# Performance work log

Hardware: AMD Instinct MI355X
Metric: run time of the kernel (lower is better)

## Reference

```python
import jax, jax.numpy as jnp
import numpy as np

D_IN = 512
D_OUT = 512


def setup_inputs() -> dict:
    key = jax.random.key(0)
    ks = jax.random.split(key, 7)
    B, S = 4, 4096
    sc = 1.0 / np.sqrt(D_IN)
    return {
        "x": jax.random.normal(ks[0], (B, S, D_IN), dtype=jnp.float32),
        "Wq": jax.random.normal(ks[1], (D_IN, D_OUT), dtype=jnp.float32) * sc,
        "bq": jnp.zeros((D_OUT,), dtype=jnp.float32),
        "Wk": jax.random.normal(ks[2], (D_IN, D_OUT), dtype=jnp.float32) * sc,
        "bk": jnp.zeros((D_OUT,), dtype=jnp.float32),
        "Wv": jax.random.normal(ks[3], (D_IN, D_OUT), dtype=jnp.float32) * sc,
        "bv": jnp.zeros((D_OUT,), dtype=jnp.float32),
    }


def reference(x, Wq, bq, Wk, bk, Wv, bv):
    # Linear projections
    Q = x @ Wq + bq  # [B,S,Do]
    K = x @ Wk + bk
    V = x @ Wv + bv
    # NOTE: original torch code computes `len(K) ** 1 / 2` which is
    # (len(K)**1)/2 = batch_size / 2 due to operator precedence (not sqrt).
    scale = x.shape[0] / 2.0
    scores = jnp.einsum("bsd,btd->bst", Q, K) / scale  # [B,S,S]
    a = jax.nn.softmax(scores, axis=-1)
    Z = jnp.einsum("bst,btd->bsd", a, V)  # [B,S,Do]
    return Z
```

## Files before the change

### kernel.cpp

```cpp
#include <hip/hip_runtime.h>

typedef _Float16 h8 __attribute__((ext_vector_type(8)));
typedef float f4 __attribute__((ext_vector_type(4)));

#define MFMA16(a, b, c) __builtin_amdgcn_mfma_f32_16x16x32_f16((a), (b), (c), 0, 0, 0)

__device__ static inline void gl_lds16(const void* g, void* l) {
  __builtin_amdgcn_global_load_lds((const __attribute__((address_space(1))) unsigned int*)g,
                                   (__attribute__((address_space(3))) unsigned int*)l, 16, 0, 0);
}

__device__ static inline unsigned encf(float f) {
  unsigned u = __float_as_uint(f);
  return (u & 0x80000000u) ? ~u : (u | 0x80000000u);
}
__device__ static inline float decf(unsigned u) {
  return __uint_as_float((u & 0x80000000u) ? (u ^ 0x80000000u) : ~u);
}


__global__ void wconv_kernel(const float* __restrict__ Wq, const float* __restrict__ Wk,
                             const float* __restrict__ Wv, _Float16* __restrict__ Wt,
                             unsigned* __restrict__ mEnc) {
  int idx = blockIdx.x * 256 + threadIdx.x;
  if (idx < 16384) mEnc[idx] = 0u;
  int z = idx >> 15, rem = idx & 32767;
  int n = rem >> 6, k0 = (rem & 63) << 3;
  const float* W = (z == 0) ? Wq : (z == 1) ? Wk : Wv;
  float sc = (z == 0) ? 0.5f : 1.0f;
  h8 v;
#pragma unroll
  for (int j = 0; j < 8; ++j) v[j] = (_Float16)(W[(k0 + j) * 512 + n] * sc);
  size_t blk = (size_t)((z * 4 + (n >> 7)) * 8 + (k0 >> 6));
  int off = (n & 127) * 64 + ((((k0 >> 3) & 7) ^ (n & 7)) << 3);
  *(h8*)&Wt[blk * 8192 + off] = v;
}

__global__ void xconv_kernel(const float* __restrict__ x, _Float16* __restrict__ Ximg) {
  int idx = blockIdx.x * 256 + threadIdx.x;
  int row = idx >> 6;
  int k0 = (idx & 63) << 3;
  const float* src = &x[(size_t)row * 512 + k0];
  float4 f0 = *(const float4*)src, f1 = *(const float4*)(src + 4);
  h8 v;
  v[0] = (_Float16)f0.x; v[1] = (_Float16)f0.y; v[2] = (_Float16)f0.z; v[3] = (_Float16)f0.w;
  v[4] = (_Float16)f1.x; v[5] = (_Float16)f1.y; v[6] = (_Float16)f1.z; v[7] = (_Float16)f1.w;
  size_t blk = (size_t)((row >> 7) * 8 + (k0 >> 6));
  int off = (row & 127) * 64 + ((((k0 >> 3) & 7) ^ (row & 7)) << 3);
  *(h8*)&Ximg[blk * 8192 + off] = v;
}

__global__ __launch_bounds__(256, 3)
void proj_kernel(const _Float16* __restrict__ Ximg, const _Float16* __restrict__ Wt,
                 const float* __restrict__ bq, const float* __restrict__ bk,
                 const float* __restrict__ bv,
                 char* __restrict__ Qimg, char* __restrict__ Kimg, char* __restrict__ VTimg) {
  __shared__ _Float16 sMem[16384];
  _Float16* sA = sMem;
  _Float16* sB = sMem + 8192;
  const int tid = threadIdx.x;
  const int wave = tid >> 6, lane = tid & 63;
  const int quad = lane >> 4, lr = lane & 15;
  const int nb4 = blockIdx.x;
  const int mb = blockIdx.y;
  const int z = blockIdx.z;
  const int mbase = mb * 128, nbase = nb4 * 128;
  const int rbase = (wave & 1) * 64, cbase = (wave >> 1) * 64;
  const char* Ab = (const char*)Ximg + ((size_t)(mb * 8)) * 16384;
  const char* Bb = (const char*)Wt + ((size_t)((z * 4 + nb4) * 8)) * 16384;

  f4 acc[4][4];
#pragma unroll
  for (int i = 0; i < 4; ++i)
#pragma unroll
    for (int j = 0; j < 4; ++j) { f4 zz = {0.f, 0.f, 0.f, 0.f}; acc[i][j] = zz; }

#pragma unroll
  for (int j = 0; j < 4; ++j) {
    gl_lds16(Ab + tid * 16 + j * 4096, (char*)sA + tid * 16 + j * 4096);
    gl_lds16(Bb + tid * 16 + j * 4096, (char*)sB + tid * 16 + j * 4096);
  }

  for (int kt = 0; kt < 8; ++kt) {
    asm volatile("s_waitcnt vmcnt(0)" ::: "memory");
    __builtin_amdgcn_s_barrier();
    __builtin_amdgcn_sched_barrier(0);
    h8 a[4][2], bb[4][2];
#pragma unroll
    for (int ks = 0; ks < 2; ++ks) {
#pragma unroll
      for (int rt = 0; rt < 4; ++rt) {
        const int r = rbase + rt * 16 + lr;
        a[rt][ks] = *(const h8*)&sA[r * 64 + ((((ks << 2) | quad) ^ (lr & 7)) << 3)];
      }
#pragma unroll
      for (int ct = 0; ct < 4; ++ct) {
        const int r = cbase + ct * 16 + lr;
        bb[ct][ks] = *(const h8*)&sB[r * 64 + ((((ks << 2) | quad) ^ (lr & 7)) << 3)];
      }
    }
    asm volatile("s_waitcnt lgkmcnt(0)" ::: "memory");
    __builtin_amdgcn_s_barrier();
    __builtin_amdgcn_sched_barrier(0);
    if (kt < 7) {
#pragma unroll
      for (int j = 0; j < 4; ++j) {
        gl_lds16(Ab + (kt + 1) * 16384 + tid * 16 + j * 4096, (char*)sA + tid * 16 + j * 4096);
        gl_lds16(Bb + (kt + 1) * 16384 + tid * 16 + j * 4096, (char*)sB + tid * 16 + j * 4096);
      }
    }
    __builtin_amdgcn_s_setprio(1);
#pragma unroll
    for (int ks = 0; ks < 2; ++ks)
#pragma unroll
      for (int rt = 0; rt < 4; ++rt)
#pragma unroll
        for (int ct = 0; ct < 4; ++ct)
          acc[rt][ct] = MFMA16(a[rt][ks], bb[ct][ks], acc[rt][ct]);
    __builtin_amdgcn_s_setprio(0);
  }

  const float* bias = (z == 0) ? bq : (z == 1) ? bk : bv;
  const float bscale = (z == 0) ? 0.5f : 1.0f;
  _Float16* sC = sMem;
  __syncthreads();
#pragma unroll
  for (int ct = 0; ct < 4; ++ct) {
    const int dl = cbase + ct * 16 + lr;
    const float bb = bias[nbase + dl] * bscale;
#pragma unroll
    for (int rt = 0; rt < 4; ++rt) {
#pragma unroll
      for (int r = 0; r < 4; ++r) {
        const int sl = rbase + rt * 16 + quad * 4 + r;
        const _Float16 val = (_Float16)(acc[rt][ct][r] + bb);
        if (z == 2) {
          sC[((sl >> 6) << 13) + dl * 64 + ((((sl >> 3) & 7) ^ (dl & 7)) << 3) + (sl & 7)] = val;
        } else {
          sC[((dl >> 6) << 13) + sl * 64 + ((((dl >> 3) & 7) ^ (sl & 7)) << 3) + (dl & 7)] = val;
        }
      }
    }
  }
  __syncthreads();
  const int b_ = mbase >> 12;
  char* dst;
  if (z != 2) {
    char* img = (z == 0) ? Qimg : Kimg;
    dst = img + ((size_t)((b_ * 32 + ((mbase & 4095) >> 7)) * 8 + (nbase >> 6) + (tid >> 7))) * 16384;
  } else {
    dst = VTimg + ((size_t)((b_ * 4 + (nbase >> 7)) * 64 + ((mbase & 4095) >> 6) + (tid >> 7))) * 16384;
  }
  dst += (size_t)(tid & 127) * 128;
#pragma unroll
  for (int k = 0; k < 8; ++k)
    *(int4*)(dst + k * 16) = *(const int4*)&sC[tid * 64 + k * 8];
}

__global__ __launch_bounds__(256, 3)
void qk_kernel(const char* __restrict__ Qimg, const char* __restrict__ Kimg,
               char* __restrict__ S, unsigned* __restrict__ mEnc, int b0, int s0) {
  __shared__ _Float16 sMem[16384];
  _Float16* sA = sMem;
  _Float16* sB = sMem + 8192;
  const int tid = threadIdx.x;
  const int wave = tid >> 6, lane = tid & 63;
  const int quad = lane >> 4, lr = lane & 15;
  const int cb = blockIdx.x;
  const int rbL = blockIdx.z * gridDim.y + blockIdx.y;
  const int b = b0 + blockIdx.z;
  const int rbase = (wave & 1) * 64, cbase = (wave >> 1) * 64;
  const char* Ab = Qimg + ((size_t)((b * 32 + (s0 >> 7) + blockIdx.y) * 8)) * 16384;
  const char* Bb = Kimg + ((size_t)((b * 32 + cb) * 8)) * 16384;

  f4 acc[4][4];
#pragma unroll
  for (int i = 0; i < 4; ++i)
#pragma unroll
    for (int j = 0; j < 4; ++j) { f4 zz = {0.f, 0.f, 0.f, 0.f}; acc[i][j] = zz; }

#pragma unroll
  for (int j = 0; j < 4; ++j) {
    gl_lds16(Ab + tid * 16 + j * 4096, (char*)sA + tid * 16 + j * 4096);
    gl_lds16(Bb + tid * 16 + j * 4096, (char*)sB + tid * 16 + j * 4096);
  }

  for (int kt = 0; kt < 8; ++kt) {
    asm volatile("s_waitcnt vmcnt(0)" ::: "memory");
    __builtin_amdgcn_s_barrier();
    __builtin_amdgcn_sched_barrier(0);
    h8 a[4][2], bb[4][2];
#pragma unroll
    for (int ks = 0; ks < 2; ++ks) {
#pragma unroll
      for (int rt = 0; rt < 4; ++rt) {
        const int r = rbase + rt * 16 + lr;
        a[rt][ks] = *(const h8*)&sA[r * 64 + ((((ks << 2) | quad) ^ (lr & 7)) << 3)];
      }
#pragma unroll
      for (int ct = 0; ct < 4; ++ct) {
        const int r = cbase + ct * 16 + lr;
        bb[ct][ks] = *(const h8*)&sB[r * 64 + ((((ks << 2) | quad) ^ (lr & 7)) << 3)];
      }
    }
    asm volatile("s_waitcnt lgkmcnt(0)" ::: "memory");
    __builtin_amdgcn_s_barrier();
    __builtin_amdgcn_sched_barrier(0);
    if (kt < 7) {
#pragma unroll
      for (int j = 0; j < 4; ++j) {
        gl_lds16(Ab + (kt + 1) * 16384 + tid * 16 + j * 4096, (char*)sA + tid * 16 + j * 4096);
        gl_lds16(Bb + (kt + 1) * 16384 + tid * 16 + j * 4096, (char*)sB + tid * 16 + j * 4096);
      }
    }
    __builtin_amdgcn_s_setprio(1);
#pragma unroll
    for (int ks = 0; ks < 2; ++ks)
#pragma unroll
      for (int rt = 0; rt < 4; ++rt)
#pragma unroll
        for (int ct = 0; ct < 4; ++ct)
          acc[rt][ct] = MFMA16(a[rt][ks], bb[ct][ks], acc[rt][ct]);
    __builtin_amdgcn_s_setprio(0);
  }

  float mxv[4][4];
#pragma unroll
  for (int rt = 0; rt < 4; ++rt) {
#pragma unroll
    for (int r = 0; r < 4; ++r) {
      float mx = fmaxf(fmaxf(acc[rt][0][r], acc[rt][1][r]),
                       fmaxf(acc[rt][2][r], acc[rt][3][r]));
      mx = fmaxf(mx, __shfl_xor(mx, 1));
      mx = fmaxf(mx, __shfl_xor(mx, 2));
      mx = fmaxf(mx, __shfl_xor(mx, 4));
      mx = fmaxf(mx, __shfl_xor(mx, 8));
      mxv[rt][r] = mx;
    }
  }
  __syncthreads();
  float* rmf = (float*)sMem;
  if (lr == 0) {
#pragma unroll
    for (int rt = 0; rt < 4; ++rt)
#pragma unroll
      for (int r = 0; r < 4; ++r)
        rmf[(wave >> 1) * 128 + rbase + rt * 16 + quad * 4 + r] = mxv[rt][r];
  }
  __syncthreads();
  if (tid < 128) {
    const float v = fmaxf(rmf[tid], rmf[128 + tid]);
    atomicMax(&mEnc[b * 4096 + s0 + blockIdx.y * 128 + tid], encf(v));
  }
  __syncthreads();

  _Float16* sC = sMem;
#pragma unroll
  for (int ct = 0; ct < 4; ++ct) {
    const int tl = cbase + ct * 16 + lr;
#pragma unroll
    for (int rt = 0; rt < 4; ++rt) {
#pragma unroll
      for (int r = 0; r < 4; ++r) {
        const int sl = rbase + rt * 16 + quad * 4 + r;
        sC[((tl >> 6) << 13) + sl * 64 + ((((tl >> 3) & 7) ^ (sl & 7)) << 3) + (tl & 7)] =
            (_Float16)acc[rt][ct][r];
      }
    }
  }
  __syncthreads();
  char* dst = S + ((size_t)(rbL * 64 + cb * 2 + (tid >> 7))) * 16384 + (size_t)(tid & 127) * 128;
#pragma unroll
  for (int k = 0; k < 8; ++k)
    *(int4*)(dst + k * 16) = *(const int4*)&sC[tid * 64 + k * 8];
}

__global__ __launch_bounds__(512, 2)
void pv_kernel(const char* __restrict__ S, const char* __restrict__ VTimg,
               const unsigned* __restrict__ mEnc, float* __restrict__ out,
               int b0, int s0, int nyb, int nb) {
  __shared__ _Float16 sMem[73728];
  __shared__ float ls[64];
  const int tid = threadIdx.x;
  const int wave = tid >> 6, lane = tid & 63;
  const int quad = lane >> 4, lr = lane & 15;
  const int flat = blockIdx.x;
  int bL, yl;
  if (nb == 4) { bL = (flat & 7) >> 1; yl = ((flat >> 3) << 1) | (flat & 1); }
  else { bL = flat / nyb; yl = flat - bL * nyb; }
  const int b = b0 + bL;
  const int sbL = bL * nyb + yl;
  const int rbase = (wave & 1) * 32, cbase = (wave >> 1) * 128;
  const char* Ab = S + ((size_t)((sbL >> 1) * 64)) * 16384 + (size_t)(sbL & 1) * 8192;
  const char* Bb = VTimg + ((size_t)(b * 4) * 64) * 16384;

  const int lrow = tid >> 3;
  const float m0 = decf(mEnc[b * 4096 + s0 + yl * 64 + lrow]);
  float rs = 0.f;

  f4 acc[2][8];
#pragma unroll
  for (int i = 0; i < 2; ++i)
#pragma unroll
    for (int j = 0; j < 8; ++j) { f4 zz = {0.f, 0.f, 0.f, 0.f}; acc[i][j] = zz; }

  {
    h8 ha = *(const h8*)(Ab + tid * 16);
#pragma unroll
    for (int j = 0; j < 8; ++j)
      gl_lds16(Bb + (size_t)(j >> 1) * 1048576 + (j & 1) * 8192 + tid * 16,
               (char*)sMem + 16384 + j * 8192 + tid * 16);
    h8 w;
#pragma unroll
    for (int u = 0; u < 8; ++u) { float e = __expf((float)ha[u] - m0); w[u] = (_Float16)e; rs += e; }
    *(h8*)((char*)sMem + tid * 16) = w;
    asm volatile("s_waitcnt vmcnt(0) lgkmcnt(0)" ::: "memory");
    __builtin_amdgcn_s_barrier();
    __builtin_amdgcn_sched_barrier(0);
  }

  for (int kt = 0; kt < 64; ++kt) {
    const int cur = kt & 1;
    _Float16* sA = sMem + cur * 4096;
    _Float16* sB = sMem + 8192 + cur * 32768;
    char* sAn = (char*)sMem + (cur ^ 1) * 8192;
    char* sBn = (char*)sMem + 16384 + (cur ^ 1) * 65536;
    const bool more = (kt < 63);
    h8 han;
    if (more) {
      han = *(const h8*)(Ab + (kt + 1) * 16384 + tid * 16);
#pragma unroll
      for (int j = 0; j < 8; ++j)
        gl_lds16(Bb + (size_t)(j >> 1) * 1048576 + (size_t)(kt + 1) * 16384 + (j & 1) * 8192 + tid * 16,
                 sBn + j * 8192 + tid * 16);
    }
    {
      h8 a[2], bbf[8];
#pragma unroll
      for (int rt = 0; rt < 2; ++rt) {
        const int r = rbase + rt * 16 + lr;
        a[rt] = *(const h8*)&sA[r * 64 + (((quad) ^ (lr & 7)) << 3)];
      }
#pragma unroll
      for (int ct = 0; ct < 8; ++ct) {
        const int d = cbase + ct * 16 + lr;
        bbf[ct] = *(const h8*)&sB[d * 64 + (((quad) ^ (lr & 7)) << 3)];
      }
      __builtin_amdgcn_s_setprio(1);
#pragma unroll
      for (int rt = 0; rt < 2; ++rt)
#pragma unroll
        for (int ct = 0; ct < 8; ++ct)
          acc[rt][ct] = MFMA16(a[rt], bbf[ct], acc[rt][ct]);
      __builtin_amdgcn_s_setprio(0);
    }
    if (more) {
      h8 w;
#pragma unroll
      for (int u = 0; u < 8; ++u) { float e = __expf((float)han[u] - m0); w[u] = (_Float16)e; rs += e; }
      *(h8*)(sAn + tid * 16) = w;
    }
    {
      h8 a[2], bbf[8];
#pragma unroll
      for (int rt = 0; rt < 2; ++rt) {
        const int r = rbase + rt * 16 + lr;
        a[rt] = *(const h8*)&sA[r * 64 + (((4 | quad) ^ (lr & 7)) << 3)];
      }
#pragma unroll
      for (int ct = 0; ct < 8; ++ct) {
        const int d = cbase + ct * 16 + lr;
        bbf[ct] = *(const h8*)&sB[d * 64 + (((4 | quad) ^ (lr & 7)) << 3)];
      }
      __builtin_amdgcn_s_setprio(1);
#pragma unroll
      for (int rt = 0; rt < 2; ++rt)
#pragma unroll
        for (int ct = 0; ct < 8; ++ct)
          acc[rt][ct] = MFMA16(a[rt], bbf[ct], acc[rt][ct]);
      __builtin_amdgcn_s_setprio(0);
    }
    asm volatile("s_waitcnt vmcnt(0) lgkmcnt(0)" ::: "memory");
    __builtin_amdgcn_s_barrier();
    __builtin_amdgcn_sched_barrier(0);
  }

  rs += __shfl_xor(rs, 1); rs += __shfl_xor(rs, 2); rs += __shfl_xor(rs, 4);
  if ((tid & 7) == 0) ls[lrow] = rs;
  __syncthreads();

#pragma unroll
  for (int rt = 0; rt < 2; ++rt) {
#pragma unroll
    for (int r = 0; r < 4; ++r) {
      const int lrw = rbase + rt * 16 + quad * 4 + r;
      const int srow = s0 + yl * 64 + lrw;
      const float li = 1.0f / ls[lrw];
      float* op = &out[((size_t)b * 4096 + srow) * 512];
#pragma unroll
      for (int ct = 0; ct < 8; ++ct)
        op[cbase + ct * 16 + lr] = acc[rt][ct][r] * li;
    }
  }
}

extern "C" void kernel_launch(void* const* d_in, const int* in_sizes, int n_in,
                              void* d_out, int out_size, void* d_ws, size_t ws_size,
                              hipStream_t stream) {
  (void)in_sizes; (void)n_in; (void)out_size;
  const float* x  = (const float*)d_in[0];
  const float* Wq = (const float*)d_in[1];
  const float* bq = (const float*)d_in[2];
  const float* Wk = (const float*)d_in[3];
  const float* bk = (const float*)d_in[4];
  const float* Wv = (const float*)d_in[5];
  const float* bv = (const float*)d_in[6];
  float* out = (float*)d_out;
  char* ws = (char*)d_ws;
  char* Qimg  = ws;
  char* Kimg  = ws + ((size_t)16 << 20);
  char* VTimg = ws + ((size_t)32 << 20);
  _Float16* Wt = (_Float16*)(ws + ((size_t)48 << 20));
  unsigned* mEnc = (unsigned*)(ws + ((size_t)50 << 20) - 65536);
  _Float16* Ximg = (_Float16*)(ws + ((size_t)50 << 20));
  char* Simg   = ws + ((size_t)66 << 20);

  wconv_kernel<<<dim3(384), dim3(256), 0, stream>>>(Wq, Wk, Wv, Wt, mEnc);
  xconv_kernel<<<dim3(4096), dim3(256), 0, stream>>>(x, Ximg);
  proj_kernel<<<dim3(4, 128, 3), dim3(256), 0, stream>>>(Ximg, Wt, bq, bk, bv, Qimg, Kimg, VTimg);

  const size_t avail = ws_size > ((size_t)66 << 20) ? ws_size - ((size_t)66 << 20) : 0;
  int nchunk, nb, Ms;
  if      (avail >= ((size_t)128 << 20)) { nchunk = 1;  nb = 4; Ms = 4096; }
  else if (avail >= ((size_t)64  << 20)) { nchunk = 2;  nb = 2; Ms = 4096; }
  else if (avail >= ((size_t)32  << 20)) { nchunk = 4;  nb = 1; Ms = 4096; }
  else if (avail >= ((size_t)16  << 20)) { nchunk = 8;  nb = 1; Ms = 2048; }
  else if (avail >= ((size_t)8   << 20)) { nchunk = 16; nb = 1; Ms = 1024; }
  else                                   { nchunk = 32; nb = 1; Ms = 512;  }
  const int chunksPerBatch = 4096 / Ms;
  const int nyb = Ms / 64;

  for (int c = 0; c < nchunk; ++c) {
    int b0, s0;
    if (nb > 1 || Ms == 4096) { b0 = c * nb; s0 = 0; }
    else { b0 = c / chunksPerBatch; s0 = (c % chunksPerBatch) * Ms; }
    qk_kernel<<<dim3(32, Ms / 128, nb), dim3(256), 0, stream>>>(Qimg, Kimg, Simg, mEnc, b0, s0);
    pv_kernel<<<dim3(nb * nyb), dim3(512), 0, stream>>>(Simg, VTimg, mEnc, out, b0, s0, nyb, nb);
  }
}
```

Measured before the change: 378.4 us.

## Double-buffer LDS tiles in projection and QK GEMM kernels

Doubles the shared-memory allocation in proj_kernel and qk_kernel so the next K-tile is loaded into a second buffer while the current one is read and multiplied. This drops one barrier per iteration and lets global-to-LDS loads overlap the LDS reads and MFMA work. In exchange, LDS use per block doubles to 64 KB and the launch-bounds occupancy hint falls from 3 to 2 blocks per CU, which may reduce latency hiding across blocks.

```diff
diff --git a/kernel.cpp b/kernel.cpp
--- a/kernel.cpp
+++ b/kernel.cpp
@@ -50,14 +50,12 @@
   *(h8*)&Ximg[blk * 8192 + off] = v;
 }
 
-__global__ __launch_bounds__(256, 3)
+__global__ __launch_bounds__(256, 2)
 void proj_kernel(const _Float16* __restrict__ Ximg, const _Float16* __restrict__ Wt,
                  const float* __restrict__ bq, const float* __restrict__ bk,
                  const float* __restrict__ bv,
                  char* __restrict__ Qimg, char* __restrict__ Kimg, char* __restrict__ VTimg) {
-  __shared__ _Float16 sMem[16384];
-  _Float16* sA = sMem;
-  _Float16* sB = sMem + 8192;
+  __shared__ _Float16 sMem[32768];
   const int tid = threadIdx.x;
   const int wave = tid >> 6, lane = tid & 63;
   const int quad = lane >> 4, lr = lane & 15;
@@ -77,14 +75,24 @@
 
 #pragma unroll
   for (int j = 0; j < 4; ++j) {
-    gl_lds16(Ab + tid * 16 + j * 4096, (char*)sA + tid * 16 + j * 4096);
-    gl_lds16(Bb + tid * 16 + j * 4096, (char*)sB + tid * 16 + j * 4096);
-  }
+    gl_lds16(Ab + tid * 16 + j * 4096, (char*)sMem + tid * 16 + j * 4096);
+    gl_lds16(Bb + tid * 16 + j * 4096, (char*)sMem + 16384 + tid * 16 + j * 4096);
+  }
+  asm volatile("s_waitcnt vmcnt(0)" ::: "memory");
+  __builtin_amdgcn_s_barrier();
+  __builtin_amdgcn_sched_barrier(0);
 
   for (int kt = 0; kt < 8; ++kt) {
-    asm volatile("s_waitcnt vmcnt(0)" ::: "memory");
-    __builtin_amdgcn_s_barrier();
-    __builtin_amdgcn_sched_barrier(0);
+    _Float16* sA = sMem + (kt & 1) * 16384;
+    _Float16* sB = sA + 8192;
+    char* nbuf = (char*)sMem + (((kt & 1) ^ 1)) * 32768;
+    if (kt < 7) {
+#pragma unroll
+      for (int j = 0; j < 4; ++j) {
+        gl_lds16(Ab + (kt + 1) * 16384 + tid * 16 + j * 4096, nbuf + tid * 16 + j * 4096);
+        gl_lds16(Bb + (kt + 1) * 16384 + tid * 16 + j * 4096, nbuf + 16384 + tid * 16 + j * 4096);
+      }
+    }
     h8 a[4][2], bb[4][2];
 #pragma unroll
     for (int ks = 0; ks < 2; ++ks) {
@@ -100,15 +108,7 @@
       }
     }
     asm volatile("s_waitcnt lgkmcnt(0)" ::: "memory");
-    __builtin_amdgcn_s_barrier();
-    __builtin_amdgcn_sched_barrier(0);
-    if (kt < 7) {
-#pragma unroll
-      for (int j = 0; j < 4; ++j) {
-        gl_lds16(Ab + (kt + 1) * 16384 + tid * 16 + j * 4096, (char*)sA + tid * 16 + j * 4096);
-        gl_lds16(Bb + (kt + 1) * 16384 + tid * 16 + j * 4096, (char*)sB + tid * 16 + j * 4096);
-      }
-    }
+    __builtin_amdgcn_sched_barrier(0);
     __builtin_amdgcn_s_setprio(1);
 #pragma unroll
     for (int ks = 0; ks < 2; ++ks)
@@ -118,12 +118,14 @@
         for (int ct = 0; ct < 4; ++ct)
           acc[rt][ct] = MFMA16(a[rt][ks], bb[ct][ks], acc[rt][ct]);
     __builtin_amdgcn_s_setprio(0);
+    asm volatile("s_waitcnt vmcnt(0)" ::: "memory");
+    __builtin_amdgcn_s_barrier();
+    __builtin_amdgcn_sched_barrier(0);
   }
 
   const float* bias = (z == 0) ? bq : (z == 1) ? bk : bv;
   const float bscale = (z == 0) ? 0.5f : 1.0f;
   _Float16* sC = sMem;
-  __syncthreads();
 #pragma unroll
   for (int ct = 0; ct < 4; ++ct) {
     const int dl = cbase + ct * 16 + lr;
@@ -157,12 +159,10 @@
     *(int4*)(dst + k * 16) = *(const int4*)&sC[tid * 64 + k * 8];
 }
 
-__global__ __launch_bounds__(256, 3)
+__global__ __launch_bounds__(256, 2)
 void qk_kernel(const char* __restrict__ Qimg, const char* __restrict__ Kimg,
                char* __restrict__ S, unsigned* __restrict__ mEnc, int b0, int s0) {
-  __shared__ _Float16 sMem[16384];
-  _Float16* sA = sMem;
-  _Float16* sB = sMem + 8192;
+  __shared__ _Float16 sMem[32768];
   const int tid = threadIdx.x;
   const int wave = tid >> 6, lane = tid & 63;
   const int quad = lane >> 4, lr = lane & 15;
@@ -181,14 +181,24 @@
 
 #pragma unroll
   for (int j = 0; j < 4; ++j) {
-    gl_lds16(Ab + tid * 16 + j * 4096, (char*)sA + tid * 16 + j * 4096);
-    gl_lds16(Bb + tid * 16 + j * 4096, (char*)sB + tid * 16 + j * 4096);
-  }
+    gl_lds16(Ab + tid * 16 + j * 4096, (char*)sMem + tid * 16 + j * 4096);
+    gl_lds16(Bb + tid * 16 + j * 4096, (char*)sMem + 16384 + tid * 16 + j * 4096);
+  }
+  asm volatile("s_waitcnt vmcnt(0)" ::: "memory");
+  __builtin_amdgcn_s_barrier();
+  __builtin_amdgcn_sched_barrier(0);
 
   for (int kt = 0; kt < 8; ++kt) {
-    asm volatile("s_waitcnt vmcnt(0)" ::: "memory");
-    __builtin_amdgcn_s_barrier();
-    __builtin_amdgcn_sched_barrier(0);
+    _Float16* sA = sMem + (kt & 1) * 16384;
+    _Float16* sB = sA + 8192;
+    char* nbuf = (char*)sMem + (((kt & 1) ^ 1)) * 32768;
+    if (kt < 7) {
+#pragma unroll
+      for (int j = 0; j < 4; ++j) {
+        gl_lds16(Ab + (kt + 1) * 16384 + tid * 16 + j * 4096, nbuf + tid * 16 + j * 4096);
+        gl_lds16(Bb + (kt + 1) * 16384 + tid * 16 + j * 4096, nbuf + 16384 + tid * 16 + j * 4096);
+      }
+    }
     h8 a[4][2], bb[4][2];
 #pragma unroll
     for (int ks = 0; ks < 2; ++ks) {
@@ -204,15 +214,7 @@
       }
     }
     asm volatile("s_waitcnt lgkmcnt(0)" ::: "memory");
-    __builtin_amdgcn_s_barrier();
-    __builtin_amdgcn_sched_barrier(0);
-    if (kt < 7) {
-#pragma unroll
-      for (int j = 0; j < 4; ++j) {
-        gl_lds16(Ab + (kt + 1) * 16384 + tid * 16 + j * 4096, (char*)sA + tid * 16 + j * 4096);
-        gl_lds16(Bb + (kt + 1) * 16384 + tid * 16 + j * 4096, (char*)sB + tid * 16 + j * 4096);
-      }
-    }
+    __builtin_amdgcn_sched_barrier(0);
     __builtin_amdgcn_s_setprio(1);
 #pragma unroll
     for (int ks = 0; ks < 2; ++ks)
@@ -222,6 +224,9 @@
         for (int ct = 0; ct < 4; ++ct)
           acc[rt][ct] = MFMA16(a[rt][ks], bb[ct][ks], acc[rt][ct]);
     __builtin_amdgcn_s_setprio(0);
+    asm volatile("s_waitcnt vmcnt(0)" ::: "memory");
+    __builtin_amdgcn_s_barrier();
+    __builtin_amdgcn_sched_barrier(0);
   }
 
   float mxv[4][4];
@@ -238,7 +243,6 @@
       mxv[rt][r] = mx;
     }
   }
-  __syncthreads();
   float* rmf = (float*)sMem;
   if (lr == 0) {
 #pragma unroll
```

After: 390.0 us. +3.1%, slower.
